# Performance work log

Measured on AMD Instinct MI355X. Metric: run time of the kernel, lower is better.

Reference implementation:

```python
import jax, jax.numpy as jnp
import numpy as np

IN_F = 4096
OUT_F = 4096
BITS = 8
EPS = 1e-5
BATCH, SEQ = 4, 2048


def setup_inputs() -> dict:
    key = jax.random.key(0)
    k1, k2, k3 = jax.random.split(key, 3)
    bound = 1.0 / np.sqrt(IN_F)
    x = jax.random.normal(k1, (BATCH, SEQ, IN_F), dtype=jnp.float32)
    weight = jax.random.uniform(k2, (OUT_F, IN_F), dtype=jnp.float32, minval=-bound, maxval=bound)
    bias = jax.random.uniform(k3, (OUT_F,), dtype=jnp.float32, minval=-bound, maxval=bound)
    return {"x": x, "weight": weight, "bias": bias}


def _ste_round_clip(v, lo, hi):
    # round+clip with straight-through estimator
    q = jnp.clip(jnp.round(v), lo, hi)
    return v + jax.lax.stop_gradient(q - v)


def reference(x, weight, bias):
    q = jnp.float32(2 ** (BITS - 1))  # 128 for int8
    # weight ternarization: absmean scale, round to {-1,0,1}
    w_scale = jnp.maximum(jnp.mean(jnp.abs(weight)), EPS)
    w_q = _ste_round_clip(weight / w_scale, -1.0, 1.0)  # ternary [O,I]
    # activation int8 quantization: absmax scale over whole tensor (dim=None)
    gamma = jnp.maximum(jnp.max(jnp.abs(x)), EPS)
    x_q = _ste_round_clip(x * (q / gamma), -q, q - 1.0)  # int8 range values
    # integer-domain matmul then dequantize
    out = jnp.einsum('bsi,oi->bso', x_q, w_q) * (gamma * w_scale / q)
    return out + bias
```

## Files before the change

kernel.cpp:

```cpp
#include <hip/hip_runtime.h>
#include <stdint.h>

#define GLOBAL_AS __attribute__((address_space(1)))
#define LDS_AS __attribute__((address_space(3)))

typedef int v4i  __attribute__((ext_vector_type(4)));
typedef int v16i __attribute__((ext_vector_type(16)));

static constexpr int M = 8192;
static constexpr int N = 4096;
static constexpr int K = 4096;
static constexpr float F_EPS = 1e-5f;

__global__ void init_kernel(unsigned* gmax, double* gsum) {
    if (threadIdx.x == 0) { *gmax = 0u; *gsum = 0.0; }
}

__global__ void absmax_kernel(const float4* __restrict__ x, int n4, unsigned* __restrict__ gmax) {
    float m = 0.f;
    int stride = gridDim.x * blockDim.x;
    for (int i = blockIdx.x * blockDim.x + threadIdx.x; i < n4; i += stride) {
        float4 v = x[i];
        m = fmaxf(m, fmaxf(fmaxf(fabsf(v.x), fabsf(v.y)), fmaxf(fabsf(v.z), fabsf(v.w))));
    }
#pragma unroll
    for (int off = 32; off > 0; off >>= 1) m = fmaxf(m, __shfl_down(m, off, 64));
    __shared__ float red[4];
    if ((threadIdx.x & 63) == 0) red[threadIdx.x >> 6] = m;
    __syncthreads();
    if (threadIdx.x == 0) {
        m = fmaxf(fmaxf(red[0], red[1]), fmaxf(red[2], red[3]));
        atomicMax(gmax, __float_as_uint(m));
    }
}

__global__ void wsum_kernel(const float4* __restrict__ w, int n4, double* __restrict__ gsum) {
    double s = 0.0;
    int stride = gridDim.x * blockDim.x;
    for (int i = blockIdx.x * blockDim.x + threadIdx.x; i < n4; i += stride) {
        float4 v = w[i];
        s += (double)fabsf(v.x);
        s += (double)fabsf(v.y);
        s += (double)fabsf(v.z);
        s += (double)fabsf(v.w);
    }
#pragma unroll
    for (int off = 32; off > 0; off >>= 1) s += __shfl_down(s, off, 64);
    __shared__ double red[4];
    if ((threadIdx.x & 63) == 0) red[threadIdx.x >> 6] = s;
    __syncthreads();
    if (threadIdx.x == 0) {
        s = red[0] + red[1] + red[2] + red[3];
        atomicAdd(gsum, s);
    }
}

__global__ void quantx_kernel(const float4* __restrict__ x, int* __restrict__ xq, int n4,
                              const unsigned* __restrict__ gmax) {
    float gamma = fmaxf(__uint_as_float(*gmax), F_EPS);
    float s = 128.f / gamma;
    int stride = gridDim.x * blockDim.x;
    for (int i = blockIdx.x * blockDim.x + threadIdx.x; i < n4; i += stride) {
        float4 v = x[i];
        int q0 = min(127, max(-128, (int)rintf(v.x * s)));
        int q1 = min(127, max(-128, (int)rintf(v.y * s)));
        int q2 = min(127, max(-128, (int)rintf(v.z * s)));
        int q3 = min(127, max(-128, (int)rintf(v.w * s)));
        xq[i] = (q0 & 255) | ((q1 & 255) << 8) | ((q2 & 255) << 16) | (q3 << 24);
    }
}

__global__ void quantw_kernel(const float4* __restrict__ w, int* __restrict__ wq, int n4,
                              const double* __restrict__ gsum) {
    float wscale = (float)fmax(*gsum * (1.0 / ((double)N * (double)K)), (double)F_EPS);
    int stride = gridDim.x * blockDim.x;
    for (int i = blockIdx.x * blockDim.x + threadIdx.x; i < n4; i += stride) {
        float4 v = w[i];
        int q0 = min(1, max(-1, (int)rintf(v.x / wscale)));
        int q1 = min(1, max(-1, (int)rintf(v.y / wscale)));
        int q2 = min(1, max(-1, (int)rintf(v.z / wscale)));
        int q3 = min(1, max(-1, (int)rintf(v.w / wscale)));
        wq[i] = (q0 & 255) | ((q1 & 255) << 8) | ((q2 & 255) << 16) | (q3 << 24);
    }
}

__global__ __launch_bounds__(256) void gemm_kernel(
    const int8_t* __restrict__ xq, const int8_t* __restrict__ wq,
    const float* __restrict__ bias, const unsigned* __restrict__ gmax,
    const double* __restrict__ gsum, float* __restrict__ out) {

    __shared__ __align__(16) int8_t As[128 * 128];
    __shared__ __align__(16) int8_t Bs[128 * 128];

    const int t = threadIdx.x;
    const int lane = t & 63;
    const int wv = t >> 6;
    const int half = lane >> 5;
    const int lr = lane & 31;
    const int wrow0 = (wv >> 1) * 64;
    const int wcol0 = (wv & 1) * 64;
    const int m0 = blockIdx.x * 128;
    const int n0 = blockIdx.y * 128;

    const float gamma = fmaxf(__uint_as_float(*gmax), F_EPS);
    const float wscale = (float)fmax(*gsum * (1.0 / ((double)N * (double)K)), (double)F_EPS);
    const float scale = gamma * wscale * (1.f / 128.f);

    const GLOBAL_AS int8_t* aBase[4];
    const GLOBAL_AS int8_t* bBase[4];
    int ldsOff[4];
#pragma unroll
    for (int i = 0; i < 4; ++i) {
        int idx = i * 256 + t;
        int r = idx >> 3;
        int c = idx & 7;
        int cg = c ^ (r & 7);
        aBase[i] = (const GLOBAL_AS int8_t*)(xq + (size_t)(m0 + r) * K + cg * 16);
        bBase[i] = (const GLOBAL_AS int8_t*)(wq + (size_t)(n0 + r) * K + cg * 16);
        ldsOff[i] = idx * 16;
    }

    v16i acc[2][2];
#pragma unroll
    for (int mt = 0; mt < 2; ++mt)
#pragma unroll
        for (int nt = 0; nt < 2; ++nt)
#pragma unroll
            for (int e = 0; e < 16; ++e) acc[mt][nt][e] = 0;

    const int aRow[2] = {wrow0 + lr, wrow0 + 32 + lr};
    const int bRow[2] = {wcol0 + lr, wcol0 + 32 + lr};

    for (int kt = 0; kt < K; kt += 128) {
#pragma unroll
        for (int i = 0; i < 4; ++i) {
            __builtin_amdgcn_global_load_lds((const GLOBAL_AS void*)(aBase[i] + kt),
                                             (LDS_AS void*)&As[ldsOff[i]], 16, 0, 0);
            __builtin_amdgcn_global_load_lds((const GLOBAL_AS void*)(bBase[i] + kt),
                                             (LDS_AS void*)&Bs[ldsOff[i]], 16, 0, 0);
        }
        __builtin_amdgcn_s_waitcnt(0);
        __syncthreads();

#pragma unroll
        for (int ks = 0; ks < 4; ++ks) {
            v4i a[2], b[2];
#pragma unroll
            for (int mt = 0; mt < 2; ++mt) {
                int r = aRow[mt];
                int cblk = (ks * 2 + half) ^ (r & 7);
                a[mt] = *(const v4i*)&As[r * 128 + cblk * 16];
            }
#pragma unroll
            for (int nt = 0; nt < 2; ++nt) {
                int r = bRow[nt];
                int cblk = (ks * 2 + half) ^ (r & 7);
                b[nt] = *(const v4i*)&Bs[r * 128 + cblk * 16];
            }
#pragma unroll
            for (int mt = 0; mt < 2; ++mt)
#pragma unroll
                for (int nt = 0; nt < 2; ++nt)
                    acc[mt][nt] = __builtin_amdgcn_mfma_i32_32x32x32_i8(a[mt], b[nt], acc[mt][nt], 0, 0, 0);
        }
        __syncthreads();
    }

#pragma unroll
    for (int mt = 0; mt < 2; ++mt) {
#pragma unroll
        for (int nt = 0; nt < 2; ++nt) {
            int col = n0 + wcol0 + nt * 32 + lr;
            float bv = bias[col];
#pragma unroll
            for (int reg = 0; reg < 16; ++reg) {
                int row = m0 + wrow0 + mt * 32 + 4 * half + (reg & 3) + 8 * (reg >> 2);
                out[(size_t)row * N + col] = (float)acc[mt][nt][reg] * scale + bv;
            }
        }
    }
}

extern "C" void kernel_launch(void* const* d_in, const int* in_sizes, int n_in,
                              void* d_out, int out_size, void* d_ws, size_t ws_size,
                              hipStream_t stream) {
    const float* x = (const float*)d_in[0];
    const float* w = (const float*)d_in[1];
    const float* bias = (const float*)d_in[2];
    float* out = (float*)d_out;

    unsigned* gmax = (unsigned*)d_ws;
    double* gsum = (double*)((char*)d_ws + 8);
    int8_t* xq = (int8_t*)d_ws + 16;
    int8_t* wq = xq + (size_t)M * K;

    hipLaunchKernelGGL(init_kernel, dim3(1), dim3(64), 0, stream, gmax, gsum);
    hipLaunchKernelGGL(absmax_kernel, dim3(1024), dim3(256), 0, stream,
                       (const float4*)x, M * K / 4, gmax);
    hipLaunchKernelGGL(wsum_kernel, dim3(512), dim3(256), 0, stream,
                       (const float4*)w, N * K / 4, gsum);
    hipLaunchKernelGGL(quantx_kernel, dim3(2048), dim3(256), 0, stream,
                       (const float4*)x, (int*)xq, M * K / 4, gmax);
    hipLaunchKernelGGL(quantw_kernel, dim3(1024), dim3(256), 0, stream,
                       (const float4*)w, (int*)wq, N * K / 4, gsum);
    hipLaunchKernelGGL(gemm_kernel, dim3(M / 128, N / 128), dim3(256), 0, stream,
                       xq, wq, bias, gmax, gsum, out);
}
```

Before: 495.0 us.

## Merge prep kernels and use double-buffered 256x256 int8 GEMM tiles

Merges the absmax and weight-sum reductions into one launch that writes per-block partials, and adds a one-block finalize kernel that computes the scales, so the atomics and init kernel go away. The two quantize kernels are also merged into one launch. The GEMM moves to 256x256 block tiles with a 4x4 MFMA grid per wave, K-steps of 64, double-buffered LDS and a rotated layout. This raises data reuse and overlaps the loads with compute, at the cost of more accumulator registers and lower occupancy (launch_bounds 256,1) on a grid of only 512 blocks.

```diff
diff --git a/kernel.cpp b/kernel.cpp
--- a/kernel.cpp
+++ b/kernel.cpp
@@ -12,169 +12,208 @@
 static constexpr int K = 4096;
 static constexpr float F_EPS = 1e-5f;
 
-__global__ void init_kernel(unsigned* gmax, double* gsum) {
-    if (threadIdx.x == 0) { *gmax = 0u; *gsum = 0.0; }
-}
-
-__global__ void absmax_kernel(const float4* __restrict__ x, int n4, unsigned* __restrict__ gmax) {
+
+__global__ void reduce_kernel(const float4* __restrict__ x, const float4* __restrict__ w,
+                              float* __restrict__ pmax, double* __restrict__ psum) {
+    const int b = blockIdx.x;
+    const int t = threadIdx.x;
+    if (b < 1024) {
+        float m = 0.f;
+        const int n4 = M * K / 4;
+        for (int i = b * 256 + t; i < n4; i += 1024 * 256) {
+            float4 v = x[i];
+            m = fmaxf(m, fmaxf(fmaxf(fabsf(v.x), fabsf(v.y)), fmaxf(fabsf(v.z), fabsf(v.w))));
+        }
+#pragma unroll
+        for (int off = 32; off > 0; off >>= 1) m = fmaxf(m, __shfl_down(m, off, 64));
+        __shared__ float red[4];
+        if ((t & 63) == 0) red[t >> 6] = m;
+        __syncthreads();
+        if (t == 0) pmax[b] = fmaxf(fmaxf(red[0], red[1]), fmaxf(red[2], red[3]));
+    } else {
+        double s = 0.0;
+        const int n4 = N * K / 4;
+        for (int i = (b - 1024) * 256 + t; i < n4; i += 512 * 256) {
+            float4 v = w[i];
+            s += (double)fabsf(v.x);
+            s += (double)fabsf(v.y);
+            s += (double)fabsf(v.z);
+            s += (double)fabsf(v.w);
+        }
+#pragma unroll
+        for (int off = 32; off > 0; off >>= 1) s += __shfl_down(s, off, 64);
+        __shared__ double dred[4];
+        if ((t & 63) == 0) dred[t >> 6] = s;
+        __syncthreads();
+        if (t == 0) psum[b - 1024] = dred[0] + dred[1] + dred[2] + dred[3];
+    }
+}
+
+__global__ void finalize_kernel(float* __restrict__ wssc, const float* __restrict__ pmax,
+                                const double* __restrict__ psum) {
+    const int t = threadIdx.x;
     float m = 0.f;
-    int stride = gridDim.x * blockDim.x;
-    for (int i = blockIdx.x * blockDim.x + threadIdx.x; i < n4; i += stride) {
-        float4 v = x[i];
-        m = fmaxf(m, fmaxf(fmaxf(fabsf(v.x), fabsf(v.y)), fmaxf(fabsf(v.z), fabsf(v.w))));
-    }
+    for (int i = t; i < 1024; i += 256) m = fmaxf(m, pmax[i]);
 #pragma unroll
     for (int off = 32; off > 0; off >>= 1) m = fmaxf(m, __shfl_down(m, off, 64));
+    double s = psum[t] + psum[t + 256];
+#pragma unroll
+    for (int off = 32; off > 0; off >>= 1) s += __shfl_down(s, off, 64);
     __shared__ float red[4];
-    if ((threadIdx.x & 63) == 0) red[threadIdx.x >> 6] = m;
+    __shared__ double dred[4];
+    if ((t & 63) == 0) { red[t >> 6] = m; dred[t >> 6] = s; }
     __syncthreads();
-    if (threadIdx.x == 0) {
-        m = fmaxf(fmaxf(red[0], red[1]), fmaxf(red[2], red[3]));
-        atomicMax(gmax, __float_as_uint(m));
-    }
-}
-
-__global__ void wsum_kernel(const float4* __restrict__ w, int n4, double* __restrict__ gsum) {
-    double s = 0.0;
-    int stride = gridDim.x * blockDim.x;
-    for (int i = blockIdx.x * blockDim.x + threadIdx.x; i < n4; i += stride) {
-        float4 v = w[i];
-        s += (double)fabsf(v.x);
-        s += (double)fabsf(v.y);
-        s += (double)fabsf(v.z);
-        s += (double)fabsf(v.w);
-    }
-#pragma unroll
-    for (int off = 32; off > 0; off >>= 1) s += __shfl_down(s, off, 64);
-    __shared__ double red[4];
-    if ((threadIdx.x & 63) == 0) red[threadIdx.x >> 6] = s;
-    __syncthreads();
-    if (threadIdx.x == 0) {
-        s = red[0] + red[1] + red[2] + red[3];
-        atomicAdd(gsum, s);
-    }
-}
-
-__global__ void quantx_kernel(const float4* __restrict__ x, int* __restrict__ xq, int n4,
-                              const unsigned* __restrict__ gmax) {
-    float gamma = fmaxf(__uint_as_float(*gmax), F_EPS);
-    float s = 128.f / gamma;
-    int stride = gridDim.x * blockDim.x;
-    for (int i = blockIdx.x * blockDim.x + threadIdx.x; i < n4; i += stride) {
-        float4 v = x[i];
-        int q0 = min(127, max(-128, (int)rintf(v.x * s)));
-        int q1 = min(127, max(-128, (int)rintf(v.y * s)));
-        int q2 = min(127, max(-128, (int)rintf(v.z * s)));
-        int q3 = min(127, max(-128, (int)rintf(v.w * s)));
-        xq[i] = (q0 & 255) | ((q1 & 255) << 8) | ((q2 & 255) << 16) | (q3 << 24);
-    }
-}
-
-__global__ void quantw_kernel(const float4* __restrict__ w, int* __restrict__ wq, int n4,
-                              const double* __restrict__ gsum) {
-    float wscale = (float)fmax(*gsum * (1.0 / ((double)N * (double)K)), (double)F_EPS);
-    int stride = gridDim.x * blockDim.x;
-    for (int i = blockIdx.x * blockDim.x + threadIdx.x; i < n4; i += stride) {
-        float4 v = w[i];
-        int q0 = min(1, max(-1, (int)rintf(v.x / wscale)));
-        int q1 = min(1, max(-1, (int)rintf(v.y / wscale)));
-        int q2 = min(1, max(-1, (int)rintf(v.z / wscale)));
-        int q3 = min(1, max(-1, (int)rintf(v.w / wscale)));
-        wq[i] = (q0 & 255) | ((q1 & 255) << 8) | ((q2 & 255) << 16) | (q3 << 24);
-    }
-}
-
-__global__ __launch_bounds__(256) void gemm_kernel(
+    if (t == 0) {
+        float gamma = fmaxf(fmaxf(fmaxf(red[0], red[1]), fmaxf(red[2], red[3])), F_EPS);
+        double sum = dred[0] + dred[1] + dred[2] + dred[3];
+        float wscale = (float)fmax(sum * (1.0 / ((double)N * (double)K)), (double)F_EPS);
+        wssc[0] = 128.f / gamma;
+        wssc[1] = wscale;
+        wssc[2] = gamma * wscale / 128.f;
+    }
+}
+
+__global__ void quant_kernel(const float4* __restrict__ x, const float4* __restrict__ w,
+                             int* __restrict__ xq, int* __restrict__ wq,
+                             const float* __restrict__ wssc) {
+    const int b = blockIdx.x;
+    const int t = threadIdx.x;
+    if (b < 2048) {
+        const float s = wssc[0];
+        const int n4 = M * K / 4;
+        for (int i = b * 256 + t; i < n4; i += 2048 * 256) {
+            float4 v = x[i];
+            int q0 = min(127, max(-128, (int)rintf(v.x * s)));
+            int q1 = min(127, max(-128, (int)rintf(v.y * s)));
+            int q2 = min(127, max(-128, (int)rintf(v.z * s)));
+            int q3 = min(127, max(-128, (int)rintf(v.w * s)));
+            xq[i] = (q0 & 255) | ((q1 & 255) << 8) | ((q2 & 255) << 16) | (q3 << 24);
+        }
+    } else {
+        const float ws = wssc[1];
+        const int n4 = N * K / 4;
+        for (int i = (b - 2048) * 256 + t; i < n4; i += 1024 * 256) {
+            float4 v = w[i];
+            int q0 = min(1, max(-1, (int)rintf(v.x / ws)));
+            int q1 = min(1, max(-1, (int)rintf(v.y / ws)));
+            int q2 = min(1, max(-1, (int)rintf(v.z / ws)));
+            int q3 = min(1, max(-1, (int)rintf(v.w / ws)));
+            wq[i] = (q0 & 255) | ((q1 & 255) << 8) | ((q2 & 255) << 16) | (q3 << 24);
+        }
+    }
+}
+
+__global__ __launch_bounds__(256, 1) void gemm_kernel(
     const int8_t* __restrict__ xq, const int8_t* __restrict__ wq,
-    const float* __restrict__ bias, const unsigned* __restrict__ gmax,
-    const double* __restrict__ gsum, float* __restrict__ out) {
-
-    __shared__ __align__(16) int8_t As[128 * 128];
-    __shared__ __align__(16) int8_t Bs[128 * 128];
+    const float* __restrict__ bias, const float* __restrict__ wssc,
+    float* __restrict__ out) {
+
+    __shared__ __align__(16) int8_t As0[256 * 64];
+    __shared__ __align__(16) int8_t As1[256 * 64];
+    __shared__ __align__(16) int8_t Bs0[256 * 64];
+    __shared__ __align__(16) int8_t Bs1[256 * 64];
 
     const int t = threadIdx.x;
     const int lane = t & 63;
     const int wv = t >> 6;
     const int half = lane >> 5;
     const int lr = lane & 31;
-    const int wrow0 = (wv >> 1) * 64;
-    const int wcol0 = (wv & 1) * 64;
-    const int m0 = blockIdx.x * 128;
-    const int n0 = blockIdx.y * 128;
-
-    const float gamma = fmaxf(__uint_as_float(*gmax), F_EPS);
-    const float wscale = (float)fmax(*gsum * (1.0 / ((double)N * (double)K)), (double)F_EPS);
-    const float scale = gamma * wscale * (1.f / 128.f);
-
-    const GLOBAL_AS int8_t* aBase[4];
-    const GLOBAL_AS int8_t* bBase[4];
-    int ldsOff[4];
-#pragma unroll
-    for (int i = 0; i < 4; ++i) {
-        int idx = i * 256 + t;
-        int r = idx >> 3;
-        int c = idx & 7;
-        int cg = c ^ (r & 7);
-        aBase[i] = (const GLOBAL_AS int8_t*)(xq + (size_t)(m0 + r) * K + cg * 16);
-        bBase[i] = (const GLOBAL_AS int8_t*)(wq + (size_t)(n0 + r) * K + cg * 16);
-        ldsOff[i] = idx * 16;
-    }
-
-    v16i acc[2][2];
-#pragma unroll
-    for (int mt = 0; mt < 2; ++mt)
-#pragma unroll
-        for (int nt = 0; nt < 2; ++nt)
+    const int wrow0 = (wv >> 1) * 128;
+    const int wcol0 = (wv & 1) * 128;
+    const int m0 = blockIdx.x * 256;
+    const int n0 = blockIdx.y * 256;
+
+    const GLOBAL_AS int8_t* aSrc[4];
+    const GLOBAL_AS int8_t* bSrc[4];
+    int sLds[4];
+#pragma unroll
+    for (int j = 0; j < 4; ++j) {
+        int idx = j * 256 + t;
+        int c = idx >> 6;
+        int s = idx & 63;
+        int k = s >> 4;
+        int rho = ((s & 15) - 4 * k) & 15;
+        int row = c * 16 + rho;
+        aSrc[j] = (const GLOBAL_AS int8_t*)(xq + (size_t)(m0 + row) * K + k * 16);
+        bSrc[j] = (const GLOBAL_AS int8_t*)(wq + (size_t)(n0 + row) * K + k * 16);
+        sLds[j] = idx * 16;
+    }
+
+    int aOff[2][4], bOff[2][4];
+#pragma unroll
+    for (int ks = 0; ks < 2; ++ks) {
+        int k = ks * 2 + half;
+#pragma unroll
+        for (int q = 0; q < 4; ++q) {
+            int ra = wrow0 + q * 32 + lr;
+            aOff[ks][q] = (ra >> 4) * 1024 + k * 256 + (((ra & 15) + 4 * k) & 15) * 16;
+            int rb = wcol0 + q * 32 + lr;
+            bOff[ks][q] = (rb >> 4) * 1024 + k * 256 + (((rb & 15) + 4 * k) & 15) * 16;
+        }
+    }
+
+    v16i acc[4][4];
+#pragma unroll
+    for (int mt = 0; mt < 4; ++mt)
+#pragma unroll
+        for (int nt = 0; nt < 4; ++nt)
 #pragma unroll
             for (int e = 0; e < 16; ++e) acc[mt][nt][e] = 0;
 
-    const int aRow[2] = {wrow0 + lr, wrow0 + 32 + lr};
-    const int bRow[2] = {wcol0 + lr, wcol0 + 32 + lr};
-
-    for (int kt = 0; kt < K; kt += 128) {
-#pragma unroll
-        for (int i = 0; i < 4; ++i) {
-            __builtin_amdgcn_global_load_lds((const GLOBAL_AS void*)(aBase[i] + kt),
-                                             (LDS_AS void*)&As[ldsOff[i]], 16, 0, 0);
-            __builtin_amdgcn_global_load_lds((const GLOBAL_AS void*)(bBase[i] + kt),
-                                             (LDS_AS void*)&Bs[ldsOff[i]], 16, 0, 0);
-        }
-        __builtin_amdgcn_s_waitcnt(0);
-        __syncthreads();
-
-#pragma unroll
-        for (int ks = 0; ks < 4; ++ks) {
-            v4i a[2], b[2];
-#pragma unroll
-            for (int mt = 0; mt < 2; ++mt) {
-                int r = aRow[mt];
-                int cblk = (ks * 2 + half) ^ (r & 7);
-                a[mt] = *(const v4i*)&As[r * 128 + cblk * 16];
-            }
-#pragma unroll
-            for (int nt = 0; nt < 2; ++nt) {
-                int r = bRow[nt];
-                int cblk = (ks * 2 + half) ^ (r & 7);
-                b[nt] = *(const v4i*)&Bs[r * 128 + cblk * 16];
-            }
-#pragma unroll
-            for (int mt = 0; mt < 2; ++mt)
-#pragma unroll
-                for (int nt = 0; nt < 2; ++nt)
+    auto stage = [&](int kt, int8_t* A, int8_t* B) {
+#pragma unroll
+        for (int j = 0; j < 4; ++j) {
+            __builtin_amdgcn_global_load_lds((const GLOBAL_AS void*)(aSrc[j] + kt),
+                                             (LDS_AS void*)(A + sLds[j]), 16, 0, 0);
+            __builtin_amdgcn_global_load_lds((const GLOBAL_AS void*)(bSrc[j] + kt),
+                                             (LDS_AS void*)(B + sLds[j]), 16, 0, 0);
+        }
+    };
+
+    auto compute = [&](const int8_t* A, const int8_t* B) {
+#pragma unroll
+        for (int ks = 0; ks < 2; ++ks) {
+            v4i a[4], b[4];
+#pragma unroll
+            for (int q = 0; q < 4; ++q) a[q] = *(const v4i*)(A + aOff[ks][q]);
+#pragma unroll
+            for (int q = 0; q < 4; ++q) b[q] = *(const v4i*)(B + bOff[ks][q]);
+#pragma unroll
+            for (int mt = 0; mt < 4; ++mt)
+#pragma unroll
+                for (int nt = 0; nt < 4; ++nt)
                     acc[mt][nt] = __builtin_amdgcn_mfma_i32_32x32x32_i8(a[mt], b[nt], acc[mt][nt], 0, 0, 0);
         }
-        __syncthreads();
-    }
-
-#pragma unroll
-    for (int mt = 0; mt < 2; ++mt) {
-#pragma unroll
-        for (int nt = 0; nt < 2; ++nt) {
-            int col = n0 + wcol0 + nt * 32 + lr;
-            float bv = bias[col];
+    };
+
+    constexpr int NIT = K / 64;
+    stage(0, As0, Bs0);
+    __syncthreads();
+#pragma unroll 1
+    for (int it = 0; it < NIT - 2; it += 2) {
+        stage((it + 1) * 64, As1, Bs1);
+        compute(As0, Bs0);
+        __syncthreads();
+        stage((it + 2) * 64, As0, Bs0);
+        compute(As1, Bs1);
+        __syncthreads();
+    }
+    stage((NIT - 1) * 64, As1, Bs1);
+    compute(As0, Bs0);
+    __syncthreads();
+    compute(As1, Bs1);
+
+    const float scale = wssc[2];
+#pragma unroll
+    for (int nt = 0; nt < 4; ++nt) {
+        int col = n0 + wcol0 + nt * 32 + lr;
+        float bv = bias[col];
+#pragma unroll
+        for (int mt = 0; mt < 4; ++mt) {
+            int rb = m0 + wrow0 + mt * 32 + 4 * half;
 #pragma unroll
             for (int reg = 0; reg < 16; ++reg) {
-                int row = m0 + wrow0 + mt * 32 + 4 * half + (reg & 3) + 8 * (reg >> 2);
+                int row = rb + (reg & 3) + 8 * (reg >> 2);
                 out[(size_t)row * N + col] = (float)acc[mt][nt][reg] * scale + bv;
             }
         }
@@ -189,20 +228,17 @@
     const float* bias = (const float*)d_in[2];
     float* out = (float*)d_out;
 
-    unsigned* gmax = (unsigned*)d_ws;
-    double* gsum = (double*)((char*)d_ws + 8);
-    int8_t* xq = (int8_t*)d_ws + 16;
+    float* wssc = (float*)d_ws;
+    float* pmax = (float*)((char*)d_ws + 256);
+    double* psum = (double*)((char*)d_ws + 4352);
+    int8_t* xq = (int8_t*)d_ws + 16384;
     int8_t* wq = xq + (size_t)M * K;
 
-    hipLaunchKernelGGL(init_kernel, dim3(1), dim3(64), 0, stream, gmax, gsum);
-    hipLaunchKernelGGL(absmax_kernel, dim3(1024), dim3(256), 0, stream,
-                       (const float4*)x, M * K / 4, gmax);
-    hipLaunchKernelGGL(wsum_kernel, dim3(512), dim3(256), 0, stream,
-                       (const float4*)w, N * K / 4, gsum);
-    hipLaunchKernelGGL(quantx_kernel, dim3(2048), dim3(256), 0, stream,
-                       (const float4*)x, (int*)xq, M * K / 4, gmax);
-    hipLaunchKernelGGL(quantw_kernel, dim3(1024), dim3(256), 0, stream,
-                       (const float4*)w, (int*)wq, N * K / 4, gsum);
-    hipLaunchKernelGGL(gemm_kernel, dim3(M / 128, N / 128), dim3(256), 0, stream,
-                       xq, wq, bias, gmax, gsum, out);
-}
+    hipLaunchKernelGGL(reduce_kernel, dim3(1536), dim3(256), 0, stream,
+                       (const float4*)x, (const float4*)w, pmax, psum);
+    hipLaunchKernelGGL(finalize_kernel, dim3(1), dim3(256), 0, stream, wssc, pmax, psum);
+    hipLaunchKernelGGL(quant_kernel, dim3(3072), dim3(256), 0, stream,
+                       (const float4*)x, (const float4*)w, (int*)xq, (int*)wq, wssc);
+    hipLaunchKernelGGL(gemm_kernel, dim3(M / 256, N / 256), dim3(256), 0, stream,
+                       xq, wq, bias, wssc, out);
+}
```

Measured after the change: 516.1 us. 4.3% more time.
